# Kernel optimization log

Measured on AMD Instinct MI355X. Metric: run time of the kernel, lower is better.

## Reference

```python
import jax, jax.numpy as jnp
import numpy as np

D_MODEL = 1024
NUM_HEADS = 16
ROPE_THETA = 10000.0


def setup_inputs() -> dict:
    key = jax.random.key(0)
    ks = jax.random.split(key, 5)
    B, S, D = 4, 2048, D_MODEL
    std = (2.0 / (D * D)) ** 0.5
    return {
        "x": jax.random.normal(ks[0], (B, S, D), dtype=jnp.float32),
        "Wq": jax.random.normal(ks[1], (D, D), dtype=jnp.float32) * std,
        "Wk": jax.random.normal(ks[2], (D, D), dtype=jnp.float32) * std,
        "Wv": jax.random.normal(ks[3], (D, D), dtype=jnp.float32) * std,
        "Wo": jax.random.normal(ks[4], (D, D), dtype=jnp.float32) * std,
    }


def _apply_rope(t, sin, cos):
    # t: [B, H, S, d_k]; sin/cos: [S, d_k//2] (broadcast over B, H)
    e = t[..., 0::2]
    o = t[..., 1::2]
    rot = jnp.stack((e * cos - o * sin, e * sin + o * cos), axis=-1)
    return rot.reshape(t.shape)  # interleave back to d_k


def reference(x, Wq, Wk, Wv, Wo):
    B, S, D = x.shape
    H = NUM_HEADS
    dk = D // H

    def proj(W):
        y = jnp.einsum('bsd,ed->bse', x, W)  # Linear: weight is [out, in]
        return y.reshape(B, S, H, dk).transpose(0, 2, 1, 3)  # [B,H,S,dk]

    q, k, v = proj(Wq), proj(Wk), proj(Wv)

    # RoPE cache (token_positions = arange(S))
    half = dk // 2
    inv_freq = 1.0 / (ROPE_THETA ** (jnp.arange(half, dtype=jnp.float32) * 2.0 / dk))
    angles = jnp.arange(S, dtype=jnp.float32)[:, None] * inv_freq[None, :]  # [S, half]
    sin, cos = jnp.sin(angles), jnp.cos(angles)
    q = _apply_rope(q, sin, cos)
    k = _apply_rope(k, sin, cos)

    # scaled dot-product attention with causal mask
    scores = jnp.einsum('bhqd,bhkd->bhqk', q, k) / jnp.sqrt(jnp.float32(dk))
    causal = jnp.tril(jnp.ones((S, S), dtype=bool))
    scores = jnp.where(causal, scores, jnp.finfo(scores.dtype).min)
    p = jax.nn.softmax(scores, axis=-1)
    out = jnp.einsum('bhqk,bhkd->bhqd', p, v)  # [B,H,S,dk]

    out = out.transpose(0, 2, 1, 3).reshape(B, S, D)
    return jnp.einsum('bsd,ed->bse', out, Wo)
```

## Files before the change

kernel.cpp:

```cpp
#include <hip/hip_runtime.h>

typedef unsigned short u16;
typedef unsigned int   u32;

typedef short    short8 __attribute__((ext_vector_type(8)));
typedef __bf16   bf16x8 __attribute__((ext_vector_type(8)));
typedef _Float16 half8  __attribute__((ext_vector_type(8)));
typedef float    f32x4  __attribute__((ext_vector_type(4)));

#define S_LEN   2048
#define DM      1024
#define NHEAD   16
#define DK      64
#define BH_TOT  64
#define M_TOK   8192
#define KDIM    1024

__device__ __forceinline__ u16 f2bf(float f) {
    u32 u = __builtin_bit_cast(u32, f);
    u += 0x7FFFu + ((u >> 16) & 1u);
    return (u16)(u >> 16);
}
__device__ __forceinline__ f32x4 mfma_bf16(short8 a, short8 b, f32x4 c) {
    return __builtin_amdgcn_mfma_f32_16x16x32_bf16(
        __builtin_bit_cast(bf16x8, a), __builtin_bit_cast(bf16x8, b), c, 0, 0, 0);
}
__device__ __forceinline__ f32x4 mfma_f16(half8 a, half8 b, f32x4 c) {
    return __builtin_amdgcn_mfma_f32_16x16x32_f16(a, b, c, 0, 0, 0);
}
__device__ __forceinline__ u32 pk_f16(float a, float b) {
    return __builtin_bit_cast(u32, __builtin_amdgcn_cvt_pkrtz(a, b));
}
__device__ __forceinline__ void gl_lds16(const void* g, void* l) {
    __builtin_amdgcn_global_load_lds(
        (const __attribute__((address_space(1))) u32*)g,
        (__attribute__((address_space(3))) u32*)l, 16, 0, 0);
}
__device__ __forceinline__ void bar_raw() { asm volatile("s_barrier" ::: "memory"); }
__device__ __forceinline__ void wait_vm4() { asm volatile("s_waitcnt vmcnt(4)" ::: "memory"); }
__device__ __forceinline__ void wait_vm0() { asm volatile("s_waitcnt vmcnt(0)" ::: "memory"); }

__device__ __forceinline__ int perm_inv(int rc) {
    const int nt = rc >> 4, mid = (rc >> 2) & 3, r = rc & 3;
    return 32 * (nt >> 1) + 8 * mid + 4 * (nt & 1) + r;
}

__global__ void cvt_all(const float4* __restrict__ x,  const float4* __restrict__ Wq,
                        const float4* __restrict__ Wk, const float4* __restrict__ Wv,
                        const float4* __restrict__ Wo,
                        uint2* __restrict__ oX, uint2* __restrict__ oWcat,
                        uint2* __restrict__ oWo,
                        float* __restrict__ sT, float* __restrict__ cT) {
    const int i = blockIdx.x * 256 + threadIdx.x;
    if (i < 3145728) {
        const float4* in;
        uint2* out;
        if (i < 2097152) {
            in = x + i;  out = oX + i;
        } else {
            const int j = i - 2097152;
            const int w = j >> 18, k = j & 262143;
            in  = (w == 0 ? Wq : w == 1 ? Wk : w == 2 ? Wv : Wo) + k;
            out = (w < 3) ? (oWcat + w * 262144 + k) : (oWo + k);
        }
        float4 f = *in;
        uint2 o;
        o.x = (u32)f2bf(f.x) | ((u32)f2bf(f.y) << 16);
        o.y = (u32)f2bf(f.z) | ((u32)f2bf(f.w) << 16);
        *out = o;
    } else {
        const int idx = i - 3145728;
        const float fi = expf(-(float)(idx >> 11) * 0.287823136624255f);
        const float ang = (float)(idx & 2047) * fi;
        sT[idx] = sinf(ang);
        cT[idx] = cosf(ang);
    }
}

template <int MODE>
__global__ __launch_bounds__(256)
void gemm_nt(const u16* __restrict__ A, const u16* __restrict__ Bw,
             u16* __restrict__ oQ, u16* __restrict__ oK, u16* __restrict__ oVt,
             float* __restrict__ oF,
             const float* __restrict__ ropeS, const float* __restrict__ ropeC) {
    __shared__ u16 As[2][128 * 32];
    __shared__ u16 Bs[2][128 * 32];
    const int tid  = threadIdx.x;
    const int wave = tid >> 6, lane = tid & 63;
    const int quad = lane >> 4, l15 = lane & 15;
    const int wr = wave >> 1, wc = wave & 1;
    const int NX  = (MODE == 0) ? 24 : 8;
    const int lin = (int)blockIdx.x + NX * (int)blockIdx.y;
    const int xcd = lin & 7, idx = lin >> 3;
    const int mbase = (xcd * 8 + idx / NX) * 128;
    const int nbase = (idx % NX) * 128;

    f32x4 acc[4][4];
#pragma unroll
    for (int i = 0; i < 4; i++)
#pragma unroll
        for (int j = 0; j < 4; j++) acc[i][j] = (f32x4)0.0f;

    const int srow0 = wave * 32 + (lane >> 2);
    const int srow1 = srow0 + 16;
    const int scolb = ((lane & 3) ^ ((lane >> 3) & 3)) * 16;
    const int ldsOff = wave * 2048 + lane * 16;
    const u16* gA0 = A  + (size_t)(mbase + srow0) * KDIM;
    const u16* gA1 = A  + (size_t)(mbase + srow1) * KDIM;
    const u16* gB0 = Bw + (size_t)(nbase + srow0) * KDIM;
    const u16* gB1 = Bw + (size_t)(nbase + srow1) * KDIM;
    const int koffq = (quad ^ ((l15 >> 1) & 3)) * 8;

    gl_lds16((const char*)gA0 + scolb, (char*)As[0] + ldsOff);
    gl_lds16((const char*)gA1 + scolb, (char*)As[0] + ldsOff + 1024);
    gl_lds16((const char*)gB0 + scolb, (char*)Bs[0] + ldsOff);
    gl_lds16((const char*)gB1 + scolb, (char*)Bs[0] + ldsOff + 1024);

    const int KT = KDIM / 32;
    for (int kt = 0; kt < KT; kt++) {
        const int cur = kt & 1, nxt = cur ^ 1;
        const int kkn = ((kt + 1 < KT) ? (kt + 1) : kt) * 32;
        bar_raw();
        gl_lds16((const char*)(gA0 + kkn) + scolb, (char*)As[nxt] + ldsOff);
        gl_lds16((const char*)(gA1 + kkn) + scolb, (char*)As[nxt] + ldsOff + 1024);
        gl_lds16((const char*)(gB0 + kkn) + scolb, (char*)Bs[nxt] + ldsOff);
        gl_lds16((const char*)(gB1 + kkn) + scolb, (char*)Bs[nxt] + ldsOff + 1024);
        wait_vm4();
        bar_raw();

        short8 af[4], bf[4];
#pragma unroll
        for (int mt = 0; mt < 4; mt++)
            af[mt] = *(const short8*)&As[cur][(wr * 64 + mt * 16 + l15) * 32 + koffq];
#pragma unroll
        for (int nt = 0; nt < 4; nt++)
            bf[nt] = *(const short8*)&Bs[cur][(wc * 64 + nt * 16 + l15) * 32 + koffq];
#pragma unroll
        for (int mt = 0; mt < 4; mt++)
#pragma unroll
            for (int nt = 0; nt < 4; nt++)
                acc[mt][nt] = mfma_bf16(af[mt], bf[nt], acc[mt][nt]);
    }
    wait_vm0();

    const int proj_blk = (MODE == 0) ? (nbase >> 10) : 2;

    const float* sB[4];
    const float* cB[4];
    if (MODE == 0 && proj_blk < 2) {
#pragma unroll
        for (int nt = 0; nt < 4; nt++) {
            const int fi = nt * 8 + (l15 >> 1);
            sB[nt] = ropeS + fi * 2048;
            cB[nt] = ropeC + fi * 2048;
        }
    }
    const int par = l15 & 1;

#pragma unroll
    for (int mt = 0; mt < 4; mt++) {
#pragma unroll
        for (int nt = 0; nt < 4; nt++) {
            const int n  = nbase + wc * 64 + nt * 16 + l15;
            const int mb = mbase + wr * 64 + mt * 16 + quad * 4;
            f32x4 v = acc[mt][nt];
            if (MODE == 0) {
                const int e = n & 1023;
                const int h = e >> 6, d = e & 63;
                if (proj_blk == 2) {
                    const int b_ = mb >> 11, s = mb & 2047;
                    const int bh = b_ * NHEAD + h;
                    uint2 pk;
                    pk.x = pk_f16(v[0], v[1]);
                    pk.y = pk_f16(v[2], v[3]);
                    *(uint2*)&oVt[((size_t)bh * DK + d) * S_LEN + s] = pk;
                } else {
                    u16* dst = (proj_blk == 0) ? oQ : oK;
                    float vp[4];
#pragma unroll
                    for (int r = 0; r < 4; r++) vp[r] = __shfl_xor(v[r], 1);
                    const int b_ = mb >> 11, s0 = mb & 2047;
                    const int bh = b_ * NHEAD + h;
                    const f32x4 sn = *(const f32x4*)(sB[nt] + s0);
                    const f32x4 cs = *(const f32x4*)(cB[nt] + s0);
#pragma unroll
                    for (int r = 0; r < 4; r++) {
                        const float res = par ? (vp[r] * sn[r] + v[r] * cs[r])
                                              : (v[r] * cs[r] - vp[r] * sn[r]);
                        dst[((size_t)bh * S_LEN + (s0 + r)) * DK + d] = f2bf(res);
                    }
                }
            } else {
#pragma unroll
                for (int r = 0; r < 4; r++)
                    oF[(size_t)(mb + r) * DM + n] = v[r];
            }
        }
    }
}

__global__ __launch_bounds__(256)
void flash_attn(const u16* __restrict__ Q, const u16* __restrict__ K,
                const u16* __restrict__ Vt, u16* __restrict__ Oc) {
    __shared__ u16 Ks[2][64 * 64];
    __shared__ u16 Vs[2][64 * 64];
    const int lin = (int)blockIdx.x + 64 * (int)blockIdx.y;
    const int xcd = lin & 7, idx = lin >> 3;
    const int bh  = xcd * 8 + (idx & 7);
    const int qt  = 15 - (idx >> 3);
    const int tid  = threadIdx.x;
    const int wave = tid >> 6, lane = tid & 63;
    const int quad = lane >> 4, l15 = lane & 15;
    const int x7 = l15 & 7;
    const size_t headQK = (size_t)bh * S_LEN * DK;
    const size_t headVt = (size_t)bh * DK * S_LEN;
    const int b = bh >> 4, h = bh & 15;
    const float SCL = 0.18033688011112042f;

    half8 ones;
#pragma unroll
    for (int j = 0; j < 8; j++) ones[j] = (_Float16)1.0f;

    const int rwl  = lane >> 3;
    const int scol = (lane & 7) ^ rwl;
    const int rc0 = wave * 16 + rwl, rc1 = rc0 + 8;
    const u16* gK0 = K  + headQK + (size_t)perm_inv(rc0) * DK + scol * 8;
    const u16* gK1 = K  + headQK + (size_t)perm_inv(rc1) * DK + scol * 8;
    const u16* gV0 = Vt + headVt + (size_t)rc0 * S_LEN + scol * 8;
    const u16* gV1 = Vt + headVt + (size_t)rc1 * S_LEN + scol * 8;
    const int ldsOff = wave * 2048 + lane * 16;
    const int koff0 = (quad ^ x7) * 8;
    const int koff1 = ((4 + quad) ^ x7) * 8;

    short8 qf[2][2];
#pragma unroll
    for (int hh = 0; hh < 2; hh++) {
        const int qrow = qt * 128 + hh * 64 + wave * 16 + l15;
        qf[hh][0] = *(const short8*)&Q[headQK + (size_t)qrow * DK + quad * 8];
        qf[hh][1] = *(const short8*)&Q[headQK + (size_t)qrow * DK + 32 + quad * 8];
    }

    float m_st[2];
    f32x4 lacc[2];
    f32x4 oacc[2][4];
#pragma unroll
    for (int hh = 0; hh < 2; hh++) {
        m_st[hh] = -__builtin_inff();
        lacc[hh] = (f32x4)0.0f;
#pragma unroll
        for (int n = 0; n < 4; n++) oacc[hh][n] = (f32x4)0.0f;
    }

    const int NT = 2 * qt + 2;
    gl_lds16(gK0, (char*)Ks[0] + ldsOff);
    gl_lds16(gK1, (char*)Ks[0] + ldsOff + 1024);
    gl_lds16(gV0, (char*)Vs[0] + ldsOff);
    gl_lds16(gV1, (char*)Vs[0] + ldsOff + 1024);

    for (int kt = 0; kt < NT; kt++) {
        const int cur = kt & 1, nxt = cur ^ 1;
        bar_raw();
        {
            const int ktn = (kt + 1 < NT) ? kt + 1 : kt;
            gl_lds16(gK0 + (size_t)ktn * 64 * DK, (char*)Ks[nxt] + ldsOff);
            gl_lds16(gK1 + (size_t)ktn * 64 * DK, (char*)Ks[nxt] + ldsOff + 1024);
            gl_lds16(gV0 + ktn * 64,              (char*)Vs[nxt] + ldsOff);
            gl_lds16(gV1 + ktn * 64,              (char*)Vs[nxt] + ldsOff + 1024);
        }
        wait_vm4();
        bar_raw();

#pragma unroll
        for (int hh = 0; hh < 2; hh++) {
            if (hh == 0 && kt == 2 * qt + 1) continue;
            f32x4 sc[4];
            __builtin_amdgcn_s_setprio(1);
#pragma unroll
            for (int nt = 0; nt < 4; nt++) {
                const int rb = (nt * 16 + l15) * 64;
                short8 kf0 = *(const short8*)&Ks[cur][rb + koff0];
                short8 kf1 = *(const short8*)&Ks[cur][rb + koff1];
                f32x4 z = (f32x4)0.0f;
                z = mfma_bf16(kf0, qf[hh][0], z);
                z = mfma_bf16(kf1, qf[hh][1], z);
#pragma unroll
                for (int r = 0; r < 4; r++) z[r] *= SCL;
                sc[nt] = z;
            }
            __builtin_amdgcn_s_setprio(0);
            if (kt == 2 * qt + hh) {
                const int qloc = wave * 16 + l15;
#pragma unroll
                for (int nt = 0; nt < 4; nt++) {
                    const int kb = 32 * (nt >> 1) + 8 * quad + 4 * (nt & 1);
#pragma unroll
                    for (int r = 0; r < 4; r++)
                        if (kb + r > qloc) sc[nt][r] = -__builtin_inff();
                }
            }
            float mx0 = fmaxf(fmaxf(sc[0][0], sc[0][1]), fmaxf(sc[0][2], sc[0][3]));
            float mx1 = fmaxf(fmaxf(sc[1][0], sc[1][1]), fmaxf(sc[1][2], sc[1][3]));
            float mx2 = fmaxf(fmaxf(sc[2][0], sc[2][1]), fmaxf(sc[2][2], sc[2][3]));
            float mx3 = fmaxf(fmaxf(sc[3][0], sc[3][1]), fmaxf(sc[3][2], sc[3][3]));
            float mx = fmaxf(fmaxf(mx0, mx1), fmaxf(mx2, mx3));
            mx = fmaxf(mx, __shfl_xor(mx, 16));
            mx = fmaxf(mx, __shfl_xor(mx, 32));
            const float mn = fmaxf(m_st[hh], mx);
            const float alpha = __builtin_amdgcn_exp2f(m_st[hh] - mn);
            m_st[hh] = mn;
#pragma unroll
            for (int nt = 0; nt < 4; nt++)
#pragma unroll
                for (int r = 0; r < 4; r++)
                    sc[nt][r] = __builtin_amdgcn_exp2f(sc[nt][r] - m_st[hh]);
            u32 pw[8];
            pw[0] = pk_f16(sc[0][0], sc[0][1]); pw[1] = pk_f16(sc[0][2], sc[0][3]);
            pw[2] = pk_f16(sc[1][0], sc[1][1]); pw[3] = pk_f16(sc[1][2], sc[1][3]);
            pw[4] = pk_f16(sc[2][0], sc[2][1]); pw[5] = pk_f16(sc[2][2], sc[2][3]);
            pw[6] = pk_f16(sc[3][0], sc[3][1]); pw[7] = pk_f16(sc[3][2], sc[3][3]);
            half8 pf0 = __builtin_bit_cast(half8, *(uint4*)&pw[0]);
            half8 pf1 = __builtin_bit_cast(half8, *(uint4*)&pw[4]);
            float alr[4];
#pragma unroll
            for (int r = 0; r < 4; r++) alr[r] = __shfl(alpha, quad * 20 + r);
#pragma unroll
            for (int n = 0; n < 4; n++)
#pragma unroll
                for (int r = 0; r < 4; r++) oacc[hh][n][r] *= alr[r];
#pragma unroll
            for (int r = 0; r < 4; r++) lacc[hh][r] *= alr[r];
            __builtin_amdgcn_s_setprio(1);
#pragma unroll
            for (int c = 0; c < 2; c++) {
                const half8 pf = c ? pf1 : pf0;
                lacc[hh] = mfma_f16(pf, ones, lacc[hh]);
                const int voff = ((c * 4 + quad) ^ x7) * 8;
#pragma unroll
                for (int nt2 = 0; nt2 < 4; nt2++) {
                    half8 vf = __builtin_bit_cast(half8,
                        *(const short8*)&Vs[cur][(nt2 * 16 + l15) * 64 + voff]);
                    oacc[hh][nt2] = mfma_f16(pf, vf, oacc[hh][nt2]);
                }
            }
            __builtin_amdgcn_s_setprio(0);
        }
    }
    wait_vm0();

#pragma unroll
    for (int hh = 0; hh < 2; hh++) {
#pragma unroll
        for (int r = 0; r < 4; r++) {
            const float inv = 1.0f / lacc[hh][r];
            const int s = qt * 128 + hh * 64 + wave * 16 + quad * 4 + r;
#pragma unroll
            for (int nt2 = 0; nt2 < 4; nt2++)
                Oc[((size_t)(b * S_LEN + s)) * DM + h * 64 + nt2 * 16 + l15] =
                    f2bf(oacc[hh][nt2][r] * inv);
        }
    }
}

#define OFF_XBF   ((size_t)0)
#define OFF_WCAT  ((size_t)8388608)
#define OFF_WO    ((size_t)11534336)
#define OFF_QB    ((size_t)12582912)
#define OFF_KB    ((size_t)20971520)
#define OFF_VT    ((size_t)29360128)
#define OFF_ROPE  ((size_t)37748736)

extern "C" void kernel_launch(void* const* d_in, const int* in_sizes, int n_in,
                              void* d_out, int out_size, void* d_ws, size_t ws_size,
                              hipStream_t stream) {
    const float* x  = (const float*)d_in[0];
    const float* Wq = (const float*)d_in[1];
    const float* Wk = (const float*)d_in[2];
    const float* Wv = (const float*)d_in[3];
    const float* Wo = (const float*)d_in[4];
    u16* ws  = (u16*)d_ws;
    u16* XBF = ws + OFF_XBF;
    u16* WCA = ws + OFF_WCAT;
    u16* WOB = ws + OFF_WO;
    u16* QB  = ws + OFF_QB;
    u16* KB  = ws + OFF_KB;
    u16* VT  = ws + OFF_VT;
    float* ropeS = (float*)(ws + OFF_ROPE);
    float* ropeC = ropeS + 65536;
    u16* AT  = XBF;

    cvt_all<<<12544, 256, 0, stream>>>((const float4*)x, (const float4*)Wq,
                                       (const float4*)Wk, (const float4*)Wv,
                                       (const float4*)Wo,
                                       (uint2*)XBF, (uint2*)WCA, (uint2*)WOB,
                                       ropeS, ropeC);

    gemm_nt<0><<<dim3(24, 64), 256, 0, stream>>>(XBF, WCA, QB, KB, VT, nullptr,
                                                 ropeS, ropeC);
    flash_attn<<<dim3(64, 16), 256, 0, stream>>>(QB, KB, VT, AT);
    gemm_nt<1><<<dim3(8, 64), 256, 0, stream>>>(AT, WOB, nullptr, nullptr, nullptr,
                                                (float*)d_out, nullptr, nullptr);
}
```

Measured before the change: 270.8 us.

## Use 256x256-tile triple-buffered GEMM for fused QKV projection

Replaces the 128x128 QKV projection GEMM with a dedicated 512-thread kernel using 256x256 tiles, a three-stage LDS pipeline with split A/B staging interleaved with MFMA halves, and s_setprio around MFMA bursts. Larger tiles raise arithmetic intensity and cut global and LDS traffic per flop, and the deeper pipeline hides load latency. The cost is a smaller grid (384 blocks on 256 CUs, so a partial second wave), heavier register pressure from 128 accumulators, and 96KB of LDS per block. The output projection becomes a separate non-templated kernel.

```diff
diff --git a/kernel.cpp b/kernel.cpp
--- a/kernel.cpp
+++ b/kernel.cpp
@@ -12,8 +12,6 @@
 #define DM      1024
 #define NHEAD   16
 #define DK      64
-#define BH_TOT  64
-#define M_TOK   8192
 #define KDIM    1024
 
 __device__ __forceinline__ u16 f2bf(float f) {
@@ -77,19 +75,152 @@
     }
 }
 
-template <int MODE>
+__global__ __launch_bounds__(512, 2)
+void gemm256(const u16* __restrict__ A, const u16* __restrict__ Bw,
+             u16* __restrict__ oQ, u16* __restrict__ oK, u16* __restrict__ oVt,
+             const float* __restrict__ ropeS, const float* __restrict__ ropeC) {
+    __shared__ u16 As[3][256 * 32];
+    __shared__ u16 Bs[3][256 * 32];
+    const int tid  = threadIdx.x;
+    const int wave = tid >> 6, lane = tid & 63;
+    const int quad = lane >> 4, l15 = lane & 15;
+    const int wr = wave >> 2, wc = wave & 3;
+    const int lin = (int)blockIdx.x;
+    const int xcd = lin & 7, idx = lin >> 3;
+    const int mbase = (xcd * 4 + idx / 12) * 256;
+    const int nbase = (idx % 12) * 256;
+
+    f32x4 acc[8][4];
+#pragma unroll
+    for (int i = 0; i < 8; i++)
+#pragma unroll
+        for (int j = 0; j < 4; j++) acc[i][j] = (f32x4)0.0f;
+
+    const int srow  = tid >> 2;
+    const int scolb = ((tid & 3) ^ ((tid >> 3) & 3)) * 16;
+    const u16* gA = A  + (size_t)(mbase + srow) * KDIM;
+    const u16* gB = Bw + (size_t)(nbase + srow) * KDIM;
+    const int koffq = (quad ^ ((l15 >> 1) & 3)) * 8;
+
+#define STAGE_A(ko, bufi) do {                                            \
+        char* d_ = (char*)As[bufi] + tid * 16;                            \
+        gl_lds16((const char*)(gA + (ko)) + scolb, d_);                   \
+        gl_lds16((const char*)(gA + (ko) + (size_t)128 * KDIM) + scolb,   \
+                 d_ + 8192);                                              \
+    } while (0)
+#define STAGE_B(ko, bufi) do {                                            \
+        char* d_ = (char*)Bs[bufi] + tid * 16;                            \
+        gl_lds16((const char*)(gB + (ko)) + scolb, d_);                   \
+        gl_lds16((const char*)(gB + (ko) + (size_t)128 * KDIM) + scolb,   \
+                 d_ + 8192);                                              \
+    } while (0)
+
+    const int KT = KDIM / 32;
+    STAGE_A(0, 0);  STAGE_B(0, 0);
+    STAGE_A(32, 1); STAGE_B(32, 1);
+    wait_vm4();
+    bar_raw();
+
+    int cur = 0;
+    for (int t = 0; t < KT; t++) {
+        const bool pre = (t + 2 < KT);
+        const int stg = (cur == 0) ? 2 : cur - 1;
+        const int ko  = (t + 2) * 32;
+        if (pre) STAGE_A(ko, stg);
+        short8 af0[4], bfv[4];
+#pragma unroll
+        for (int mt = 0; mt < 4; mt++)
+            af0[mt] = *(const short8*)&As[cur][(wr * 128 + mt * 16 + l15) * 32 + koffq];
+#pragma unroll
+        for (int nt = 0; nt < 4; nt++)
+            bfv[nt] = *(const short8*)&Bs[cur][(wc * 64 + nt * 16 + l15) * 32 + koffq];
+        __builtin_amdgcn_s_setprio(1);
+#pragma unroll
+        for (int mt = 0; mt < 4; mt++)
+#pragma unroll
+            for (int nt = 0; nt < 4; nt++)
+                acc[mt][nt] = mfma_bf16(af0[mt], bfv[nt], acc[mt][nt]);
+        __builtin_amdgcn_s_setprio(0);
+        bar_raw();
+        if (pre) STAGE_B(ko, stg);
+        short8 af1[4];
+#pragma unroll
+        for (int mt = 0; mt < 4; mt++)
+            af1[mt] = *(const short8*)&As[cur][(wr * 128 + (4 + mt) * 16 + l15) * 32 + koffq];
+        __builtin_amdgcn_s_setprio(1);
+#pragma unroll
+        for (int mt = 0; mt < 4; mt++)
+#pragma unroll
+            for (int nt = 0; nt < 4; nt++)
+                acc[4 + mt][nt] = mfma_bf16(af1[mt], bfv[nt], acc[4 + mt][nt]);
+        __builtin_amdgcn_s_setprio(0);
+        if (pre) wait_vm4(); else wait_vm0();
+        bar_raw();
+        cur = (cur == 2) ? 0 : cur + 1;
+    }
+#undef STAGE_A
+#undef STAGE_B
+
+    const int proj_blk = nbase >> 10;
+
+    const float* sB[4];
+    const float* cB[4];
+    if (proj_blk < 2) {
+#pragma unroll
+        for (int nt = 0; nt < 4; nt++) {
+            const int fi = nt * 8 + (l15 >> 1);
+            sB[nt] = ropeS + fi * 2048;
+            cB[nt] = ropeC + fi * 2048;
+        }
+    }
+    const int par = l15 & 1;
+
+#pragma unroll
+    for (int mt = 0; mt < 8; mt++) {
+#pragma unroll
+        for (int nt = 0; nt < 4; nt++) {
+            const int n  = nbase + wc * 64 + nt * 16 + l15;
+            const int mb = mbase + wr * 128 + mt * 16 + quad * 4;
+            f32x4 v = acc[mt][nt];
+            const int e = n & 1023;
+            const int h = e >> 6, d = e & 63;
+            if (proj_blk == 2) {
+                const int b_ = mb >> 11, s = mb & 2047;
+                const int bh = b_ * NHEAD + h;
+                uint2 pk;
+                pk.x = pk_f16(v[0], v[1]);
+                pk.y = pk_f16(v[2], v[3]);
+                *(uint2*)&oVt[((size_t)bh * DK + d) * S_LEN + s] = pk;
+            } else {
+                u16* dst = (proj_blk == 0) ? oQ : oK;
+                float vp[4];
+#pragma unroll
+                for (int r = 0; r < 4; r++) vp[r] = __shfl_xor(v[r], 1);
+                const int b_ = mb >> 11, s0 = mb & 2047;
+                const int bh = b_ * NHEAD + h;
+                const f32x4 sn = *(const f32x4*)(sB[nt] + s0);
+                const f32x4 cs = *(const f32x4*)(cB[nt] + s0);
+#pragma unroll
+                for (int r = 0; r < 4; r++) {
+                    const float res = par ? (vp[r] * sn[r] + v[r] * cs[r])
+                                          : (v[r] * cs[r] - vp[r] * sn[r]);
+                    dst[((size_t)bh * S_LEN + (s0 + r)) * DK + d] = f2bf(res);
+                }
+            }
+        }
+    }
+}
+
 __global__ __launch_bounds__(256)
-void gemm_nt(const u16* __restrict__ A, const u16* __restrict__ Bw,
-             u16* __restrict__ oQ, u16* __restrict__ oK, u16* __restrict__ oVt,
-             float* __restrict__ oF,
-             const float* __restrict__ ropeS, const float* __restrict__ ropeC) {
+void gemm_nt1(const u16* __restrict__ A, const u16* __restrict__ Bw,
+              float* __restrict__ oF) {
     __shared__ u16 As[2][128 * 32];
     __shared__ u16 Bs[2][128 * 32];
     const int tid  = threadIdx.x;
     const int wave = tid >> 6, lane = tid & 63;
     const int quad = lane >> 4, l15 = lane & 15;
     const int wr = wave >> 1, wc = wave & 1;
-    const int NX  = (MODE == 0) ? 24 : 8;
+    const int NX  = 8;
     const int lin = (int)blockIdx.x + NX * (int)blockIdx.y;
     const int xcd = lin & 7, idx = lin >> 3;
     const int mbase = (xcd * 8 + idx / NX) * 128;
@@ -143,20 +274,6 @@
     }
     wait_vm0();
 
-    const int proj_blk = (MODE == 0) ? (nbase >> 10) : 2;
-
-    const float* sB[4];
-    const float* cB[4];
-    if (MODE == 0 && proj_blk < 2) {
-#pragma unroll
-        for (int nt = 0; nt < 4; nt++) {
-            const int fi = nt * 8 + (l15 >> 1);
-            sB[nt] = ropeS + fi * 2048;
-            cB[nt] = ropeC + fi * 2048;
-        }
-    }
-    const int par = l15 & 1;
-
 #pragma unroll
     for (int mt = 0; mt < 4; mt++) {
 #pragma unroll
@@ -164,37 +281,9 @@
             const int n  = nbase + wc * 64 + nt * 16 + l15;
             const int mb = mbase + wr * 64 + mt * 16 + quad * 4;
             f32x4 v = acc[mt][nt];
-            if (MODE == 0) {
-                const int e = n & 1023;
-                const int h = e >> 6, d = e & 63;
-                if (proj_blk == 2) {
-                    const int b_ = mb >> 11, s = mb & 2047;
-                    const int bh = b_ * NHEAD + h;
-                    uint2 pk;
-                    pk.x = pk_f16(v[0], v[1]);
-                    pk.y = pk_f16(v[2], v[3]);
-                    *(uint2*)&oVt[((size_t)bh * DK + d) * S_LEN + s] = pk;
-                } else {
-                    u16* dst = (proj_blk == 0) ? oQ : oK;
-                    float vp[4];
-#pragma unroll
-                    for (int r = 0; r < 4; r++) vp[r] = __shfl_xor(v[r], 1);
-                    const int b_ = mb >> 11, s0 = mb & 2047;
-                    const int bh = b_ * NHEAD + h;
-                    const f32x4 sn = *(const f32x4*)(sB[nt] + s0);
-                    const f32x4 cs = *(const f32x4*)(cB[nt] + s0);
-#pragma unroll
-                    for (int r = 0; r < 4; r++) {
-                        const float res = par ? (vp[r] * sn[r] + v[r] * cs[r])
-                                              : (v[r] * cs[r] - vp[r] * sn[r]);
-                        dst[((size_t)bh * S_LEN + (s0 + r)) * DK + d] = f2bf(res);
-                    }
-                }
-            } else {
-#pragma unroll
-                for (int r = 0; r < 4; r++)
-                    oF[(size_t)(mb + r) * DM + n] = v[r];
-            }
+#pragma unroll
+            for (int r = 0; r < 4; r++)
+                oF[(size_t)(mb + r) * DM + n] = v[r];
         }
     }
 }
@@ -394,9 +483,7 @@
                                        (uint2*)XBF, (uint2*)WCA, (uint2*)WOB,
                                        ropeS, ropeC);
 
-    gemm_nt<0><<<dim3(24, 64), 256, 0, stream>>>(XBF, WCA, QB, KB, VT, nullptr,
-                                                 ropeS, ropeC);
+    gemm256<<<384, 512, 0, stream>>>(XBF, WCA, QB, KB, VT, ropeS, ropeC);
     flash_attn<<<dim3(64, 16), 256, 0, stream>>>(QB, KB, VT, AT);
-    gemm_nt<1><<<dim3(8, 64), 256, 0, stream>>>(AT, WOB, nullptr, nullptr, nullptr,
-                                                (float*)d_out, nullptr, nullptr);
-}
+    gemm_nt1<<<dim3(8, 64), 256, 0, stream>>>(AT, WOB, (float*)d_out);
+}
```

New measurement: 293.5 us. 8.4% more time.
